# Optimization experiments

Hardware: AMD Instinct MI355X
Metric: run time of the kernel (lower is better)

The kernel has to match this reference:

```python
import jax, jax.numpy as jnp
import numpy as np

# Module config (from init_kwargs)
KH, KW = 3, 3          # kernel_size
SH, SW = 2, 2          # stride
PH, PW = 1, 1          # padding
EPS = 1e-8             # temperature clamp eps
DEN_EPS = 1e-12        # denominator stabilizer (hardcoded in kornia)
DN = ('NCHW', 'OIHW', 'NCHW')


def _window_grid_kernel(kh, kw):
    # window coordinates residual to window center, normalized to [-1, 1]
    ys, xs = jnp.meshgrid(jnp.arange(kh, dtype=jnp.float32),
                          jnp.arange(kw, dtype=jnp.float32), indexing='ij')
    gx = xs * (2.0 / (kw - 1)) - 1.0
    gy = ys * (2.0 / (kh - 1)) - 1.0
    return jnp.stack([gx, gy], axis=0)[:, None]  # (2,1,kh,kw), ch0=x, ch1=y


def _center_kernel(kh, kw):
    k = jnp.zeros((2, 2, kh, kw), jnp.float32)
    k = k.at[0, 0, kh // 2, kw // 2].set(1.0)
    k = k.at[1, 1, kh // 2, kw // 2].set(1.0)
    return k  # (2,2,kh,kw)


def _sum_pool(x):
    # pool_coef * avg_pool2d(count_include_pad=True) == windowed sum with zero pad
    return jax.lax.reduce_window(x, 0.0, jax.lax.add,
                                 (1, 1, KH, KW), (1, 1, SH, SW),
                                 [(0, 0), (0, 0), (PH, PH), (PW, PW)])


def setup_inputs() -> dict:
    key = jax.random.key(0)
    x = jax.random.normal(key, (8, 16, 512, 512), dtype=jnp.float32)
    temperature = jnp.ones((), dtype=jnp.float32)
    return {"x": x, "temperature": temperature}


def reference(x, temperature):
    b, c, h, w = x.shape
    xf = x.reshape(b * c, 1, h, w)

    x_exp = jnp.exp(xf / jnp.maximum(temperature, EPS))

    den = _sum_pool(x_exp) + DEN_EPS                     # (BC,1,Ho,Wo)
    resp_maxima = _sum_pool(x_exp * xf) / den            # softmax-pooled values

    # weighted sum of window-relative coordinates
    coords_num = jax.lax.conv_general_dilated(
        x_exp, _window_grid_kernel(KH, KW), (SH, SW),
        [(PH, PH), (PW, PW)], dimension_numbers=DN)      # (BC,2,Ho,Wo)

    # global grid (x, y) pixel coordinates, center-picked per window
    ys, xs = jnp.meshgrid(jnp.arange(h, dtype=jnp.float32),
                          jnp.arange(w, dtype=jnp.float32), indexing='ij')
    grid_global = jnp.stack([xs, ys], axis=0)[None]      # (1,2,h,w)
    grid_pooled = jax.lax.conv_general_dilated(
        grid_global, _center_kernel(KH, KW), (SH, SW),
        [(PH, PH), (PW, PW)], dimension_numbers=DN)      # (1,2,Ho,Wo)

    coords_max = coords_num / den + grid_pooled          # broadcast over BC

    # normalized_coordinates=True: map pixel coords to [-1, 1]
    cx = coords_max[:, 0] * (2.0 / (w - 1)) - 1.0
    cy = coords_max[:, 1] * (2.0 / (h - 1)) - 1.0
    coords_max = jnp.stack([cx, cy], axis=1)             # (BC,2,Ho,Wo)

    return coords_max, resp_maxima
```

## Files before the change

### kernel.cpp

```cpp
#include <hip/hip_runtime.h>


#define H  512
#define W  512
#define HO 256
#define WO 256
#define BC 128

__global__ __launch_bounds__(256) void casm_kernel(
    const float* __restrict__ x, const float* __restrict__ temp,
    float* __restrict__ out)
{
    int idx = blockIdx.x * 256 + threadIdx.x;
    int wo = idx & (WO - 1);
    int ho = (idx >> 8) & (HO - 1);
    int bc = idx >> 16;

    float k = 1.44269504088896340736f / fmaxf(temp[0], 1e-8f);

    const float* __restrict__ xp = x + (size_t)bc * (H * W);
    int r0 = 2 * ho - 1;
    int c0 = 2 * wo - 1;
    int cL = c0 < 0 ? 0 : c0;
    float mL = c0 < 0 ? 0.0f : 1.0f;
    int cM = 2 * wo;

    float s0 = 0.f, s1, s2;
    float colL = 0.f, colR = 0.f, numv = 0.f;

    if (r0 >= 0) {
        const float* __restrict__ row = xp + r0 * W;
        float  v0 = row[cL];
        float2 v12 = *(const float2*)(row + cM);
        float e0 = mL * __builtin_amdgcn_exp2f(k * v0);
        float e1 = __builtin_amdgcn_exp2f(k * v12.x);
        float e2 = __builtin_amdgcn_exp2f(k * v12.y);
        s0 = e0 + e1 + e2;
        colL += e0; colR += e2;
        numv = fmaf(e0, v0, fmaf(e1, v12.x, fmaf(e2, v12.y, numv)));
    }
    {
        const float* __restrict__ row = xp + (r0 + 1) * W;
        float  v0 = row[cL];
        float2 v12 = *(const float2*)(row + cM);
        float e0 = mL * __builtin_amdgcn_exp2f(k * v0);
        float e1 = __builtin_amdgcn_exp2f(k * v12.x);
        float e2 = __builtin_amdgcn_exp2f(k * v12.y);
        s1 = e0 + e1 + e2;
        colL += e0; colR += e2;
        numv = fmaf(e0, v0, fmaf(e1, v12.x, fmaf(e2, v12.y, numv)));
    }
    {
        const float* __restrict__ row = xp + (r0 + 2) * W;
        float  v0 = row[cL];
        float2 v12 = *(const float2*)(row + cM);
        float e0 = mL * __builtin_amdgcn_exp2f(k * v0);
        float e1 = __builtin_amdgcn_exp2f(k * v12.x);
        float e2 = __builtin_amdgcn_exp2f(k * v12.y);
        s2 = e0 + e1 + e2;
        colL += e0; colR += e2;
        numv = fmaf(e0, v0, fmaf(e1, v12.x, fmaf(e2, v12.y, numv)));
    }

    float den = s0 + s1 + s2 + 1e-12f;
    float inv_den = __builtin_amdgcn_rcpf(den);
    const float scale = 2.0f / 511.0f;
    float cx   = ((colR - colL) * inv_den + (float)(2 * wo)) * scale - 1.0f;
    float cy   = ((s2 - s0)    * inv_den + (float)(2 * ho)) * scale - 1.0f;
    float resp = numv * inv_den;

    size_t pix   = (size_t)ho * WO + wo;
    size_t cbase = (size_t)bc * (2 * HO * WO) + pix;
    out[cbase]           = cx;
    out[cbase + HO * WO] = cy;
    out[(size_t)BC * 2 * HO * WO + (size_t)bc * HO * WO + pix] = resp;
}

extern "C" void kernel_launch(void* const* d_in, const int* in_sizes, int n_in,
                              void* d_out, int out_size, void* d_ws, size_t ws_size,
                              hipStream_t stream) {
    const float* x    = (const float*)d_in[0];
    const float* temp = (const float*)d_in[1];
    float* out        = (float*)d_out;

    int total  = BC * HO * WO;
    int blocks = total / 256;
    casm_kernel<<<blocks, 256, 0, stream>>>(x, temp, out);
}
```

Before: 218.3 us.

## Compute two output pixels per thread with float4 loads and shuffle halo

Each thread now handles two adjacent output columns, loading four contiguous input values per row and getting the left halo element from the neighbouring lane via shuffle (falling back to a global load at wavefront edges). This removes the duplicated loads and exp evaluations of shared columns and halves the thread count. Outputs are written as nontemporal float2 stores. A block index swizzle remaps blocks, presumably for better locality across dies. The cost is more registers per thread and fewer threads.

```diff
diff --git a/kernel.cpp b/kernel.cpp
--- a/kernel.cpp
+++ b/kernel.cpp
@@ -7,73 +7,71 @@
 #define WO 256
 #define BC 128
 
+typedef float v2f __attribute__((ext_vector_type(2)));
+
 __global__ __launch_bounds__(256) void casm_kernel(
     const float* __restrict__ x, const float* __restrict__ temp,
     float* __restrict__ out)
 {
-    int idx = blockIdx.x * 256 + threadIdx.x;
-    int wo = idx & (WO - 1);
-    int ho = (idx >> 8) & (HO - 1);
-    int bc = idx >> 16;
+    int nblk = gridDim.x;
+    int bid  = blockIdx.x;
+    int swz  = (bid & 7) * (nblk >> 3) + (bid >> 3);
+
+    int idx = swz * 256 + (int)threadIdx.x;
+    int t   = idx & 127;
+    int ho  = (idx >> 7) & (HO - 1);
+    int bc  = idx >> 15;
 
     float k = 1.44269504088896340736f / fmaxf(temp[0], 1e-8f);
 
     const float* __restrict__ xp = x + (size_t)bc * (H * W);
     int r0 = 2 * ho - 1;
-    int c0 = 2 * wo - 1;
-    int cL = c0 < 0 ? 0 : c0;
-    float mL = c0 < 0 ? 0.0f : 1.0f;
-    int cM = 2 * wo;
+    int cM = 4 * t;
+    float mL = (t == 0) ? 0.0f : 1.0f;
 
-    float s0 = 0.f, s1, s2;
-    float colL = 0.f, colR = 0.f, numv = 0.f;
+    float den_a = 0.f, den_b = 0.f, cyn_a = 0.f, cyn_b = 0.f;
+    float colL_a = 0.f, colR_a = 0.f, colL_b = 0.f, colR_b = 0.f;
+    float num_a = 0.f, num_b = 0.f;
 
-    if (r0 >= 0) {
-        const float* __restrict__ row = xp + r0 * W;
-        float  v0 = row[cL];
-        float2 v12 = *(const float2*)(row + cM);
-        float e0 = mL * __builtin_amdgcn_exp2f(k * v0);
-        float e1 = __builtin_amdgcn_exp2f(k * v12.x);
-        float e2 = __builtin_amdgcn_exp2f(k * v12.y);
-        s0 = e0 + e1 + e2;
-        colL += e0; colR += e2;
-        numv = fmaf(e0, v0, fmaf(e1, v12.x, fmaf(e2, v12.y, numv)));
-    }
-    {
-        const float* __restrict__ row = xp + (r0 + 1) * W;
-        float  v0 = row[cL];
-        float2 v12 = *(const float2*)(row + cM);
-        float e0 = mL * __builtin_amdgcn_exp2f(k * v0);
-        float e1 = __builtin_amdgcn_exp2f(k * v12.x);
-        float e2 = __builtin_amdgcn_exp2f(k * v12.y);
-        s1 = e0 + e1 + e2;
-        colL += e0; colR += e2;
-        numv = fmaf(e0, v0, fmaf(e1, v12.x, fmaf(e2, v12.y, numv)));
-    }
-    {
-        const float* __restrict__ row = xp + (r0 + 2) * W;
-        float  v0 = row[cL];
-        float2 v12 = *(const float2*)(row + cM);
-        float e0 = mL * __builtin_amdgcn_exp2f(k * v0);
-        float e1 = __builtin_amdgcn_exp2f(k * v12.x);
-        float e2 = __builtin_amdgcn_exp2f(k * v12.y);
-        s2 = e0 + e1 + e2;
-        colL += e0; colR += e2;
-        numv = fmaf(e0, v0, fmaf(e1, v12.x, fmaf(e2, v12.y, numv)));
+#pragma unroll
+    for (int rr = 0; rr < 3; ++rr) {
+        if (rr == 0 && r0 < 0) continue;
+        const float* __restrict__ row = xp + (r0 + rr) * W;
+        float4 v = *(const float4*)(row + cM);
+        float vL = __shfl_up(v.w, 1);
+        if ((t & 63) == 0 && t != 0) vL = row[cM - 1];
+        float eL = mL * __builtin_amdgcn_exp2f(k * vL);
+        float e0 = __builtin_amdgcn_exp2f(k * v.x);
+        float e1 = __builtin_amdgcn_exp2f(k * v.y);
+        float e2 = __builtin_amdgcn_exp2f(k * v.z);
+        float e3 = __builtin_amdgcn_exp2f(k * v.w);
+        float rs_a = eL + e0 + e1;
+        float rs_b = e1 + e2 + e3;
+        den_a += rs_a;  den_b += rs_b;
+        if (rr == 0) { cyn_a -= rs_a; cyn_b -= rs_b; }
+        if (rr == 2) { cyn_a += rs_a; cyn_b += rs_b; }
+        colL_a += eL;  colR_a += e1;
+        colL_b += e1;  colR_b += e3;
+        num_a = fmaf(eL, vL, fmaf(e0, v.x, fmaf(e1, v.y, num_a)));
+        num_b = fmaf(e1, v.y, fmaf(e2, v.z, fmaf(e3, v.w, num_b)));
     }
 
-    float den = s0 + s1 + s2 + 1e-12f;
-    float inv_den = __builtin_amdgcn_rcpf(den);
+    float ia = __builtin_amdgcn_rcpf(den_a + 1e-12f);
+    float ib = __builtin_amdgcn_rcpf(den_b + 1e-12f);
     const float scale = 2.0f / 511.0f;
-    float cx   = ((colR - colL) * inv_den + (float)(2 * wo)) * scale - 1.0f;
-    float cy   = ((s2 - s0)    * inv_den + (float)(2 * ho)) * scale - 1.0f;
-    float resp = numv * inv_den;
+    int wo0 = 2 * t;
+    v2f vx = { ((colR_a - colL_a) * ia + (float)(2 * wo0    )) * scale - 1.0f,
+               ((colR_b - colL_b) * ib + (float)(2 * wo0 + 2)) * scale - 1.0f };
+    v2f vy = { (cyn_a * ia + (float)(2 * ho)) * scale - 1.0f,
+               (cyn_b * ib + (float)(2 * ho)) * scale - 1.0f };
+    v2f vr = { num_a * ia, num_b * ib };
 
-    size_t pix   = (size_t)ho * WO + wo;
+    size_t pix   = (size_t)ho * WO + wo0;
     size_t cbase = (size_t)bc * (2 * HO * WO) + pix;
-    out[cbase]           = cx;
-    out[cbase + HO * WO] = cy;
-    out[(size_t)BC * 2 * HO * WO + (size_t)bc * HO * WO + pix] = resp;
+    __builtin_nontemporal_store(vx, (v2f*)(out + cbase));
+    __builtin_nontemporal_store(vy, (v2f*)(out + cbase + HO * WO));
+    __builtin_nontemporal_store(vr, (v2f*)(out + (size_t)BC * 2 * HO * WO
+                                           + (size_t)bc * HO * WO + pix));
 }
 
 extern "C" void kernel_launch(void* const* d_in, const int* in_sizes, int n_in,
@@ -83,7 +81,7 @@
     const float* temp = (const float*)d_in[1];
     float* out        = (float*)d_out;
 
-    int total  = BC * HO * WO;
+    int total  = BC * HO * (WO / 2);
     int blocks = total / 256;
     casm_kernel<<<blocks, 256, 0, stream>>>(x, temp, out);
 }
```

After: 222.2 us. No clear change (+1.8%).
